# Optimization experiments

Measured on AMD Instinct MI355X. Metric: run time of the kernel, lower is better.

The kernel has to match this reference:

```python
import jax, jax.numpy as jnp
import numpy as np

N, IN_DIM, ERR_DIM, CAND, NR = 100000, 168, 24, 256, 4

def setup_inputs() -> dict:
    key = jax.random.key(0)
    k1, k2, k3, k4, k5 = jax.random.split(key, 5)
    return {
        "input": jax.random.normal(k1, (N, IN_DIM), dtype=jnp.float32),
        "error": jax.random.normal(k2, (N, ERR_DIM), dtype=jnp.float32),
        "weight_candidates": jax.random.normal(k3, (IN_DIM, CAND), dtype=jnp.float32),
        "bias_candidates": jax.random.normal(k4, (1, CAND), dtype=jnp.float32),
        "r": jax.random.uniform(k5, (NR,), dtype=jnp.float32),
    }

def reference(input, error, weight_candidates, bias_candidates, r):
    # candidates_state: [N, C] = sigmoid(X W + b)
    cand_state = jax.nn.sigmoid(input @ weight_candidates + bias_candidates)
    # E^T C: [D, C]; replaces per-(candidate,dim) tiny mm loop
    ec = jnp.einsum('nd,nc->dc', error, cand_state)
    # c^T c per candidate: [C]
    cc = jnp.sum(cand_state * cand_state, axis=0)
    # left_vector summed over dims: [C]
    left = jnp.sum(ec * ec, axis=0) / cc
    # sum over dims of e_dim^T e_dim: scalar
    ee = jnp.sum(error * error)
    # scores[idx, i] = sum_dim left - (1 - r_i) * right
    scores = left[:, None] - (1.0 - r)[None, :] * ee  # [C, NR]
    return scores
```

## Files before the change

### kernel.cpp

```cpp
#include <hip/hip_runtime.h>


#define N_ROWS 100000
#define IN_DIM 168
#define ERR_DIM 24
#define CAND 256

#define M_TILE 64
#define NT 1563
#define GRID_MAIN 512
#define XT_STRIDE 200
#define ST_STRIDE 72
#define NCOPY 8

typedef __bf16 bf16;
typedef bf16 bf16x4 __attribute__((ext_vector_type(4)));
typedef bf16 bf16x8 __attribute__((ext_vector_type(8)));
typedef float f32x4 __attribute__((ext_vector_type(4)));

#define EC_F 0
#define CC_F 49152
#define EE_F 51200
#define ZERO_N 51712
#define WP_F 51712

__device__ __forceinline__ f32x4 mfma16(bf16x8 a, bf16x8 b, f32x4 c) {
    return __builtin_amdgcn_mfma_f32_16x16x32_bf16(a, b, c, 0, 0, 0);
}

__device__ __forceinline__ float fast_sigmoid(float x) {
    return __builtin_amdgcn_rcpf(1.0f + __expf(-x));
}

__global__ __launch_bounds__(256) void prep_kernel(const float* __restrict__ W,
                                                   bf16* __restrict__ wp,
                                                   float* __restrict__ zero_region) {
    int tid = blockIdx.x * 256 + threadIdx.x;
    for (int i = tid; i < ZERO_N; i += 6144) zero_region[i] = 0.0f;
    int ct  = tid / 384;
    int rem = tid % 384;
    int kt  = rem / 64;
    int l   = rem % 64;
    int c   = ct * 16 + (l & 15);
    int k0  = kt * 32 + (l >> 4) * 8;
    bf16x8 v;
#pragma unroll
    for (int j = 0; j < 8; ++j) {
        int k = k0 + j;
        float f = (k < IN_DIM) ? W[(size_t)k * CAND + c] : 0.0f;
        v[j] = (bf16)f;
    }
    *reinterpret_cast<bf16x8*>(wp + (size_t)tid * 8) = v;
}

__global__ __launch_bounds__(256, 2) void fused_main(const float* __restrict__ X,
                                                     const float* __restrict__ E,
                                                     const float* __restrict__ B,
                                                     const bf16* __restrict__ wp,
                                                     float* __restrict__ ec_ws,
                                                     float* __restrict__ cc_ws,
                                                     float* __restrict__ ee_ws) {
    __shared__ bf16 XT[M_TILE * XT_STRIDE];
    __shared__ bf16 SigT[CAND * ST_STRIDE];
    __shared__ bf16 ET[32 * ST_STRIDE];
    __shared__ float red[8];

    const int tid  = threadIdx.x;
    const int wave = tid >> 6;
    const int lane = tid & 63;
    const int lo   = lane & 15;
    const int hi   = lane >> 4;
    const int wcol = wave * 64;

    bf16x8 wf[4][6];
#pragma unroll
    for (int cf = 0; cf < 4; ++cf)
#pragma unroll
        for (int kt = 0; kt < 6; ++kt) {
            int ct = (wcol >> 4) + cf;
            wf[cf][kt] = *reinterpret_cast<const bf16x8*>(wp + (((size_t)(ct * 6 + kt)) * 64 + lane) * 8);
        }

    float bv[4];
#pragma unroll
    for (int cf = 0; cf < 4; ++cf) bv[cf] = B[wcol + cf * 16 + lo];

    f32x4 ec_acc[2][4];
#pragma unroll
    for (int rf = 0; rf < 2; ++rf)
#pragma unroll
        for (int cf = 0; cf < 4; ++cf) ec_acc[rf][cf] = (f32x4){0.f, 0.f, 0.f, 0.f};
    float cc_acc[4] = {0.f, 0.f, 0.f, 0.f};
    float ee_acc = 0.f;

    for (int i = tid; i < 8 * ST_STRIDE; i += 256)
        ET[(24 + i / ST_STRIDE) * ST_STRIDE + (i % ST_STRIDE)] = (bf16)0.0f;
    {
        bf16x4 z = {(bf16)0.f, (bf16)0.f, (bf16)0.f, (bf16)0.f};
        for (int i = tid; i < 64 * 6; i += 256) {
            int r = i / 6, p = i % 6;
            *reinterpret_cast<bf16x4*>(&XT[r * XT_STRIDE + IN_DIM + p * 4]) = z;
        }
    }

    for (int t = blockIdx.x; t < NT; t += GRID_MAIN) {
        const int row0 = t * M_TILE;
        __syncthreads();

        f32x4 xr[11], er[2];
#pragma unroll
        for (int j = 0; j < 11; ++j) {
            int idx = tid + j * 256;
            int r = idx / 42, c4 = idx - r * 42;
            int gr = row0 + r;
            f32x4 v = {0.f, 0.f, 0.f, 0.f};
            if (idx < 2688 && gr < N_ROWS)
                v = *reinterpret_cast<const f32x4*>(X + (size_t)gr * IN_DIM + c4 * 4);
            xr[j] = v;
        }
#pragma unroll
        for (int j = 0; j < 2; ++j) {
            int idx = tid + j * 256;
            int r = idx / 6, p = idx - r * 6;
            int gr = row0 + r;
            f32x4 v = {0.f, 0.f, 0.f, 0.f};
            if (idx < 384 && gr < N_ROWS)
                v = *reinterpret_cast<const f32x4*>(E + (size_t)gr * ERR_DIM + p * 4);
            er[j] = v;
        }

#pragma unroll
        for (int j = 0; j < 11; ++j) {
            int idx = tid + j * 256;
            if (idx < 2688) {
                int r = idx / 42, c4 = idx - r * 42;
                f32x4 v = xr[j];
                bf16x4 pk = {(bf16)v.x, (bf16)v.y, (bf16)v.z, (bf16)v.w};
                *reinterpret_cast<bf16x4*>(&XT[r * XT_STRIDE + c4 * 4]) = pk;
            }
        }
#pragma unroll
        for (int j = 0; j < 2; ++j) {
            int idx = tid + j * 256;
            if (idx < 384) {
                int r = idx / 6, p = idx - r * 6;
                f32x4 v = er[j];
                ee_acc += v.x * v.x + v.y * v.y + v.z * v.z + v.w * v.w;
                int d0 = p * 4;
                ET[(d0 + 0) * ST_STRIDE + r] = (bf16)v.x;
                ET[(d0 + 1) * ST_STRIDE + r] = (bf16)v.y;
                ET[(d0 + 2) * ST_STRIDE + r] = (bf16)v.z;
                ET[(d0 + 3) * ST_STRIDE + r] = (bf16)v.w;
            }
        }
        __syncthreads();

        f32x4 acc[4][4];
#pragma unroll
        for (int mf = 0; mf < 4; ++mf)
#pragma unroll
            for (int cf = 0; cf < 4; ++cf) acc[mf][cf] = (f32x4){0.f, 0.f, 0.f, 0.f};
#pragma unroll
        for (int kt = 0; kt < 6; ++kt) {
            bf16x8 a[4];
#pragma unroll
            for (int mf = 0; mf < 4; ++mf)
                a[mf] = *reinterpret_cast<const bf16x8*>(&XT[(mf * 16 + lo) * XT_STRIDE + kt * 32 + hi * 8]);
#pragma unroll
            for (int mf = 0; mf < 4; ++mf)
#pragma unroll
                for (int cf = 0; cf < 4; ++cf)
                    acc[mf][cf] = mfma16(a[mf], wf[cf][kt], acc[mf][cf]);
        }

#pragma unroll
        for (int mf = 0; mf < 4; ++mf) {
            const int rb = row0 + mf * 16 + hi * 4;
#pragma unroll
            for (int cf = 0; cf < 4; ++cf) {
                f32x4 v = acc[mf][cf];
                float s0 = fast_sigmoid(v.x + bv[cf]);
                float s1 = fast_sigmoid(v.y + bv[cf]);
                float s2 = fast_sigmoid(v.z + bv[cf]);
                float s3 = fast_sigmoid(v.w + bv[cf]);
                if (rb + 0 >= N_ROWS) s0 = 0.0f;
                if (rb + 1 >= N_ROWS) s1 = 0.0f;
                if (rb + 2 >= N_ROWS) s2 = 0.0f;
                if (rb + 3 >= N_ROWS) s3 = 0.0f;
                cc_acc[cf] += s0 * s0 + s1 * s1 + s2 * s2 + s3 * s3;
                bf16x4 pk = {(bf16)s0, (bf16)s1, (bf16)s2, (bf16)s3};
                *reinterpret_cast<bf16x4*>(&SigT[(wcol + cf * 16 + lo) * ST_STRIDE + mf * 16 + hi * 4]) = pk;
            }
        }

#pragma unroll
        for (int kt2 = 0; kt2 < 2; ++kt2) {
            bf16x8 ea[2], sb[4];
#pragma unroll
            for (int rf = 0; rf < 2; ++rf)
                ea[rf] = *reinterpret_cast<const bf16x8*>(&ET[(rf * 16 + lo) * ST_STRIDE + kt2 * 32 + hi * 8]);
#pragma unroll
            for (int cf = 0; cf < 4; ++cf)
                sb[cf] = *reinterpret_cast<const bf16x8*>(&SigT[(wcol + cf * 16 + lo) * ST_STRIDE + kt2 * 32 + hi * 8]);
#pragma unroll
            for (int rf = 0; rf < 2; ++rf)
#pragma unroll
                for (int cf = 0; cf < 4; ++cf)
                    ec_acc[rf][cf] = mfma16(ea[rf], sb[cf], ec_acc[rf][cf]);
        }
    }

    const int copy = blockIdx.x & (NCOPY - 1);
#pragma unroll
    for (int rf = 0; rf < 2; ++rf)
#pragma unroll
        for (int cf = 0; cf < 4; ++cf)
#pragma unroll
            for (int rr = 0; rr < 4; ++rr) {
                int d = rf * 16 + hi * 4 + rr;
                if (d < ERR_DIM)
                    atomicAdd(&ec_ws[copy * (ERR_DIM * CAND) + d * CAND + wcol + cf * 16 + lo],
                              ec_acc[rf][cf][rr]);
            }
#pragma unroll
    for (int cf = 0; cf < 4; ++cf) {
        float v = cc_acc[cf];
        v += __shfl_down(v, 32);
        v += __shfl_down(v, 16);
        if (lane < 16) atomicAdd(&cc_ws[copy * CAND + wcol + cf * 16 + lane], v);
    }
#pragma unroll
    for (int off = 32; off > 0; off >>= 1) ee_acc += __shfl_down(ee_acc, off);
    if (lane == 0) red[wave] = ee_acc;
    __syncthreads();
    if (tid == 0) ee_ws[blockIdx.x] = red[0] + red[1] + red[2] + red[3];
}

__global__ __launch_bounds__(256) void finalize(const float* __restrict__ ec_ws,
                                                const float* __restrict__ cc_ws,
                                                const float* __restrict__ ee_ws,
                                                const float* __restrict__ r,
                                                float* __restrict__ out) {
    __shared__ float tmp[4];
    __shared__ float s_ee;
    int c = threadIdx.x;
    float p = ee_ws[c] + ee_ws[c + 256];
#pragma unroll
    for (int off = 32; off > 0; off >>= 1) p += __shfl_down(p, off);
    if ((c & 63) == 0) tmp[c >> 6] = p;
    __syncthreads();
    if (c == 0) s_ee = tmp[0] + tmp[1] + tmp[2] + tmp[3];
    __syncthreads();
    float ee = s_ee;
    float ccv = 0.f;
#pragma unroll
    for (int cp = 0; cp < NCOPY; ++cp) ccv += cc_ws[cp * CAND + c];
    float left = 0.f;
#pragma unroll
    for (int d = 0; d < ERR_DIM; ++d) {
        float v = 0.f;
#pragma unroll
        for (int cp = 0; cp < NCOPY; ++cp) v += ec_ws[cp * (ERR_DIM * CAND) + d * CAND + c];
        left += v * v;
    }
    left /= ccv;
#pragma unroll
    for (int i = 0; i < 4; ++i) out[c * 4 + i] = left - (1.0f - r[i]) * ee;
}

extern "C" void kernel_launch(void* const* d_in, const int* in_sizes, int n_in,
                              void* d_out, int out_size, void* d_ws, size_t ws_size,
                              hipStream_t stream) {
    const float* X = (const float*)d_in[0];
    const float* E = (const float*)d_in[1];
    const float* W = (const float*)d_in[2];
    const float* B = (const float*)d_in[3];
    const float* r = (const float*)d_in[4];

    float* wsf   = (float*)d_ws;
    float* ec_ws = wsf + EC_F;
    float* cc_ws = wsf + CC_F;
    float* ee_ws = wsf + EE_F;
    bf16*  wp    = (bf16*)(wsf + WP_F);

    prep_kernel<<<24, 256, 0, stream>>>(W, wp, wsf);
    fused_main<<<GRID_MAIN, 256, 0, stream>>>(X, E, B, wp, ec_ws, cc_ws, ee_ws);
    finalize<<<1, 256, 0, stream>>>(ec_ws, cc_ws, ee_ws, r, (float*)d_out);
}
```

Before: 166.4 us.

## Split candidate columns across four blocks per row tile to cut registers

The fused kernel now launches 1024 blocks: each of 256 row-groups is split into 4 candidate groups of 64 columns, so each wave handles 16 candidates instead of 64. This shrinks accumulators and weight fragments and allows 4 blocks per CU instead of 2, which is meant to raise occupancy. The cost is that every X and E tile is loaded and converted to bf16 four times, one per candidate group, which multiplies global read traffic for X. The ee partial sums are computed only by the first candidate group.

```diff
diff --git a/kernel.cpp b/kernel.cpp
--- a/kernel.cpp
+++ b/kernel.cpp
@@ -8,7 +8,7 @@
 
 #define M_TILE 64
 #define NT 1563
-#define GRID_MAIN 512
+#define RBLKS 256
 #define XT_STRIDE 200
 #define ST_STRIDE 72
 #define NCOPY 8
@@ -21,7 +21,7 @@
 #define EC_F 0
 #define CC_F 49152
 #define EE_F 51200
-#define ZERO_N 51712
+#define ZERO_N 51456
 #define WP_F 51712
 
 __device__ __forceinline__ f32x4 mfma16(bf16x8 a, bf16x8 b, f32x4 c) {
@@ -53,7 +53,7 @@
     *reinterpret_cast<bf16x8*>(wp + (size_t)tid * 8) = v;
 }
 
-__global__ __launch_bounds__(256, 2) void fused_main(const float* __restrict__ X,
+__global__ __launch_bounds__(256, 4) void fused_main(const float* __restrict__ X,
                                                      const float* __restrict__ E,
                                                      const float* __restrict__ B,
                                                      const bf16* __restrict__ wp,
@@ -61,36 +61,32 @@
                                                      float* __restrict__ cc_ws,
                                                      float* __restrict__ ee_ws) {
     __shared__ bf16 XT[M_TILE * XT_STRIDE];
-    __shared__ bf16 SigT[CAND * ST_STRIDE];
+    __shared__ bf16 SigT[64 * ST_STRIDE];
     __shared__ bf16 ET[32 * ST_STRIDE];
     __shared__ float red[8];
+
+    const int pid  = blockIdx.x;
+    const int cg   = (pid >> 3) >> 5;
+    const int rblk = (((pid >> 3) & 31) << 3) | (pid & 7);
 
     const int tid  = threadIdx.x;
     const int wave = tid >> 6;
     const int lane = tid & 63;
     const int lo   = lane & 15;
     const int hi   = lane >> 4;
-    const int wcol = wave * 64;
-
-    bf16x8 wf[4][6];
-#pragma unroll
-    for (int cf = 0; cf < 4; ++cf)
-#pragma unroll
-        for (int kt = 0; kt < 6; ++kt) {
-            int ct = (wcol >> 4) + cf;
-            wf[cf][kt] = *reinterpret_cast<const bf16x8*>(wp + (((size_t)(ct * 6 + kt)) * 64 + lane) * 8);
-        }
-
-    float bv[4];
-#pragma unroll
-    for (int cf = 0; cf < 4; ++cf) bv[cf] = B[wcol + cf * 16 + lo];
-
-    f32x4 ec_acc[2][4];
-#pragma unroll
-    for (int rf = 0; rf < 2; ++rf)
-#pragma unroll
-        for (int cf = 0; cf < 4; ++cf) ec_acc[rf][cf] = (f32x4){0.f, 0.f, 0.f, 0.f};
-    float cc_acc[4] = {0.f, 0.f, 0.f, 0.f};
+    const int ct   = cg * 4 + wave;
+    const int cand = ct * 16 + lo;
+
+    bf16x8 wf[6];
+#pragma unroll
+    for (int kt = 0; kt < 6; ++kt)
+        wf[kt] = *reinterpret_cast<const bf16x8*>(wp + (((size_t)(ct * 6 + kt)) * 64 + lane) * 8);
+    const float bv = B[cand];
+
+    f32x4 ec_acc[2];
+    ec_acc[0] = (f32x4){0.f, 0.f, 0.f, 0.f};
+    ec_acc[1] = (f32x4){0.f, 0.f, 0.f, 0.f};
+    float cc_acc = 0.f;
     float ee_acc = 0.f;
 
     for (int i = tid; i < 8 * ST_STRIDE; i += 256)
@@ -103,7 +99,7 @@
         }
     }
 
-    for (int t = blockIdx.x; t < NT; t += GRID_MAIN) {
+    for (int t = rblk; t < NT; t += RBLKS) {
         const int row0 = t * M_TILE;
         __syncthreads();
 
@@ -145,7 +141,8 @@
             if (idx < 384) {
                 int r = idx / 6, p = idx - r * 6;
                 f32x4 v = er[j];
-                ee_acc += v.x * v.x + v.y * v.y + v.z * v.z + v.w * v.w;
+                if (cg == 0)
+                    ee_acc += v.x * v.x + v.y * v.y + v.z * v.z + v.w * v.w;
                 int d0 = p * 4;
                 ET[(d0 + 0) * ST_STRIDE + r] = (bf16)v.x;
                 ET[(d0 + 1) * ST_STRIDE + r] = (bf16)v.y;
@@ -155,11 +152,9 @@
         }
         __syncthreads();
 
-        f32x4 acc[4][4];
-#pragma unroll
-        for (int mf = 0; mf < 4; ++mf)
-#pragma unroll
-            for (int cf = 0; cf < 4; ++cf) acc[mf][cf] = (f32x4){0.f, 0.f, 0.f, 0.f};
+        f32x4 acc[4];
+#pragma unroll
+        for (int mf = 0; mf < 4; ++mf) acc[mf] = (f32x4){0.f, 0.f, 0.f, 0.f};
 #pragma unroll
         for (int kt = 0; kt < 6; ++kt) {
             bf16x8 a[4];
@@ -168,72 +163,58 @@
                 a[mf] = *reinterpret_cast<const bf16x8*>(&XT[(mf * 16 + lo) * XT_STRIDE + kt * 32 + hi * 8]);
 #pragma unroll
             for (int mf = 0; mf < 4; ++mf)
-#pragma unroll
-                for (int cf = 0; cf < 4; ++cf)
-                    acc[mf][cf] = mfma16(a[mf], wf[cf][kt], acc[mf][cf]);
+                acc[mf] = mfma16(a[mf], wf[kt], acc[mf]);
         }
 
 #pragma unroll
         for (int mf = 0; mf < 4; ++mf) {
             const int rb = row0 + mf * 16 + hi * 4;
-#pragma unroll
-            for (int cf = 0; cf < 4; ++cf) {
-                f32x4 v = acc[mf][cf];
-                float s0 = fast_sigmoid(v.x + bv[cf]);
-                float s1 = fast_sigmoid(v.y + bv[cf]);
-                float s2 = fast_sigmoid(v.z + bv[cf]);
-                float s3 = fast_sigmoid(v.w + bv[cf]);
-                if (rb + 0 >= N_ROWS) s0 = 0.0f;
-                if (rb + 1 >= N_ROWS) s1 = 0.0f;
-                if (rb + 2 >= N_ROWS) s2 = 0.0f;
-                if (rb + 3 >= N_ROWS) s3 = 0.0f;
-                cc_acc[cf] += s0 * s0 + s1 * s1 + s2 * s2 + s3 * s3;
-                bf16x4 pk = {(bf16)s0, (bf16)s1, (bf16)s2, (bf16)s3};
-                *reinterpret_cast<bf16x4*>(&SigT[(wcol + cf * 16 + lo) * ST_STRIDE + mf * 16 + hi * 4]) = pk;
-            }
+            f32x4 v = acc[mf];
+            float s0 = fast_sigmoid(v.x + bv);
+            float s1 = fast_sigmoid(v.y + bv);
+            float s2 = fast_sigmoid(v.z + bv);
+            float s3 = fast_sigmoid(v.w + bv);
+            if (rb + 0 >= N_ROWS) s0 = 0.0f;
+            if (rb + 1 >= N_ROWS) s1 = 0.0f;
+            if (rb + 2 >= N_ROWS) s2 = 0.0f;
+            if (rb + 3 >= N_ROWS) s3 = 0.0f;
+            cc_acc += s0 * s0 + s1 * s1 + s2 * s2 + s3 * s3;
+            bf16x4 pk = {(bf16)s0, (bf16)s1, (bf16)s2, (bf16)s3};
+            *reinterpret_cast<bf16x4*>(&SigT[(wave * 16 + lo) * ST_STRIDE + mf * 16 + hi * 4]) = pk;
         }
 
 #pragma unroll
         for (int kt2 = 0; kt2 < 2; ++kt2) {
-            bf16x8 ea[2], sb[4];
-#pragma unroll
-            for (int rf = 0; rf < 2; ++rf)
-                ea[rf] = *reinterpret_cast<const bf16x8*>(&ET[(rf * 16 + lo) * ST_STRIDE + kt2 * 32 + hi * 8]);
-#pragma unroll
-            for (int cf = 0; cf < 4; ++cf)
-                sb[cf] = *reinterpret_cast<const bf16x8*>(&SigT[(wcol + cf * 16 + lo) * ST_STRIDE + kt2 * 32 + hi * 8]);
-#pragma unroll
-            for (int rf = 0; rf < 2; ++rf)
-#pragma unroll
-                for (int cf = 0; cf < 4; ++cf)
-                    ec_acc[rf][cf] = mfma16(ea[rf], sb[cf], ec_acc[rf][cf]);
-        }
-    }
-
-    const int copy = blockIdx.x & (NCOPY - 1);
+            bf16x8 ea0 = *reinterpret_cast<const bf16x8*>(&ET[(0 * 16 + lo) * ST_STRIDE + kt2 * 32 + hi * 8]);
+            bf16x8 ea1 = *reinterpret_cast<const bf16x8*>(&ET[(1 * 16 + lo) * ST_STRIDE + kt2 * 32 + hi * 8]);
+            bf16x8 sb  = *reinterpret_cast<const bf16x8*>(&SigT[(wave * 16 + lo) * ST_STRIDE + kt2 * 32 + hi * 8]);
+            ec_acc[0] = mfma16(ea0, sb, ec_acc[0]);
+            ec_acc[1] = mfma16(ea1, sb, ec_acc[1]);
+        }
+    }
+
+    const int copy = rblk & (NCOPY - 1);
 #pragma unroll
     for (int rf = 0; rf < 2; ++rf)
 #pragma unroll
-        for (int cf = 0; cf < 4; ++cf)
-#pragma unroll
-            for (int rr = 0; rr < 4; ++rr) {
-                int d = rf * 16 + hi * 4 + rr;
-                if (d < ERR_DIM)
-                    atomicAdd(&ec_ws[copy * (ERR_DIM * CAND) + d * CAND + wcol + cf * 16 + lo],
-                              ec_acc[rf][cf][rr]);
-            }
-#pragma unroll
-    for (int cf = 0; cf < 4; ++cf) {
-        float v = cc_acc[cf];
+        for (int rr = 0; rr < 4; ++rr) {
+            int d = rf * 16 + hi * 4 + rr;
+            if (d < ERR_DIM)
+                atomicAdd(&ec_ws[copy * (ERR_DIM * CAND) + d * CAND + cand], ec_acc[rf][rr]);
+        }
+    {
+        float v = cc_acc;
         v += __shfl_down(v, 32);
         v += __shfl_down(v, 16);
-        if (lane < 16) atomicAdd(&cc_ws[copy * CAND + wcol + cf * 16 + lane], v);
-    }
-#pragma unroll
-    for (int off = 32; off > 0; off >>= 1) ee_acc += __shfl_down(ee_acc, off);
-    if (lane == 0) red[wave] = ee_acc;
+        if (lane < 16) atomicAdd(&cc_ws[copy * CAND + ct * 16 + lane], v);
+    }
+    if (cg == 0) {
+#pragma unroll
+        for (int off = 32; off > 0; off >>= 1) ee_acc += __shfl_down(ee_acc, off);
+        if (lane == 0) red[wave] = ee_acc;
+    }
     __syncthreads();
-    if (tid == 0) ee_ws[blockIdx.x] = red[0] + red[1] + red[2] + red[3];
+    if (cg == 0 && tid == 0) ee_ws[rblk] = red[0] + red[1] + red[2] + red[3];
 }
 
 __global__ __launch_bounds__(256) void finalize(const float* __restrict__ ec_ws,
@@ -244,7 +225,7 @@
     __shared__ float tmp[4];
     __shared__ float s_ee;
     int c = threadIdx.x;
-    float p = ee_ws[c] + ee_ws[c + 256];
+    float p = ee_ws[c];
 #pragma unroll
     for (int off = 32; off > 0; off >>= 1) p += __shfl_down(p, off);
     if ((c & 63) == 0) tmp[c >> 6] = p;
@@ -284,6 +265,6 @@
     bf16*  wp    = (bf16*)(wsf + WP_F);
 
     prep_kernel<<<24, 256, 0, stream>>>(W, wp, wsf);
-    fused_main<<<GRID_MAIN, 256, 0, stream>>>(X, E, B, wp, ec_ws, cc_ws, ee_ws);
+    fused_main<<<4 * RBLKS, 256, 0, stream>>>(X, E, B, wp, ec_ws, cc_ws, ee_ws);
     finalize<<<1, 256, 0, stream>>>(ec_ws, cc_ws, ee_ws, r, (float*)d_out);
 }
```

New measurement: 160.4 us. 1.04x faster.
